# Performance work log

Measured on AMD Instinct MI355X. Metric: run time of the kernel, lower is better.

## Reference

```python
import jax, jax.numpy as jnp
import numpy as np

N_HEADS = 2
N_POINTS = 3
BN_EPS = 1e-5


def make_pe(C, D):
    # PositionalEncoding buffer, sliced to depth D: shape (D, C)
    pos = np.arange(D, dtype=np.float32)[:, None]
    div = np.exp(np.arange(0, C, 2, dtype=np.float32) * (-np.log(10000.0) / C))
    pe = np.zeros((D, C), dtype=np.float32)
    pe[:, 0::2] = np.sin(pos * div)
    pe[:, 1::2] = np.cos(pos * div)
    return jnp.asarray(pe)


def setup_inputs() -> dict:
    key = jax.random.key(0)
    b, c, zs, h, w = 2, 256, 32, 48, 48
    hp = N_HEADS * N_POINTS
    ks = jax.random.split(key, 8)
    features = jax.random.normal(ks[0], (b, c, zs, h, w), dtype=jnp.float32)
    # 1x1 Conv3d weights (out_ch, in_ch), no bias
    q_w = jax.random.normal(ks[1], (c, c), dtype=jnp.float32) * 0.05
    v_w = jax.random.normal(ks[2], (c, c), dtype=jnp.float32) * 0.05
    o_w = jax.random.normal(ks[3], (c, c), dtype=jnp.float32) * 0.05
    # sampling_offsets Linear: module inits weight=0, bias=[-1,-2,-3,1,2,3];
    # we add small random weight so sampling is input-dependent (non-degenerate)
    offs_w = jax.random.normal(ks[4], (hp, c), dtype=jnp.float32) * 0.02
    direction = np.array([[-1.0, -2.0, -3.0], [1.0, 2.0, 3.0]], dtype=np.float32)
    offs_b = jnp.asarray(direction.reshape(-1))
    attn_w = jax.random.normal(ks[5], (hp, c), dtype=jnp.float32) * 0.02
    attn_b = jax.random.normal(ks[6], (hp,), dtype=jnp.float32) * 0.1
    gamma = jnp.ones((c,), dtype=jnp.float32)
    beta = jnp.zeros((c,), dtype=jnp.float32)
    return {"features": features, "q_w": q_w, "v_w": v_w, "o_w": o_w,
            "offs_w": offs_w, "offs_b": offs_b, "attn_w": attn_w,
            "attn_b": attn_b, "gamma": gamma, "beta": beta}


def reference(features, q_w, v_w, o_w, offs_w, offs_b, attn_w, attn_b, gamma, beta):
    b, c, zs, h, w = features.shape
    pe = make_pe(c, zs)  # (zs, c)
    x = features + pe.T[None, :, :, None, None]  # (b,c,zs,h,w)
    # 1x1 conv3d == per-voxel channel GEMM
    q = jnp.einsum('oc,bcdhw->bodhw', q_w, x)
    v = jnp.einsum('oc,bcdhw->bodhw', v_w, x)
    # AdaptiveMaxPool1d(1) over h*w -> global spatial max; (b,zs,c)
    qp = jnp.transpose(q.max(axis=(3, 4)), (0, 2, 1))
    off = jnp.clip(qp @ offs_w.T + offs_b, 0.0, zs - 1)      # (b,zs,hp)
    attn = jax.nn.softmax(qp @ attn_w.T + attn_b, axis=-1)    # (b,zs,hp)
    lo = jnp.floor(off)
    hi = jnp.ceil(off)
    frac = off - lo
    # gather index depends only on (b,zs,hp), not (c,h,w): fold the
    # interp-weighted gather into a per-batch (zs_out, zs_in) mixing matrix.
    w_lo = attn * (1.0 - frac)
    w_hi = attn * frac
    oh_lo = jax.nn.one_hot(lo.astype(jnp.int32), zs, dtype=features.dtype)
    oh_hi = jax.nn.one_hot(hi.astype(jnp.int32), zs, dtype=features.dtype)
    M = (oh_lo * w_lo[..., None] + oh_hi * w_hi[..., None]).sum(axis=2)  # (b,zs,zs)
    samp = jnp.einsum('bzy,bcyhw->bczhw', M, v)  # (b,c,zs,h,w)
    out = jnp.einsum('oc,bcdhw->bodhw', o_w, samp)
    # BatchNorm3d, training-mode batch statistics (biased var), eps=1e-5
    mean = out.mean(axis=(0, 2, 3, 4))
    var = out.var(axis=(0, 2, 3, 4))
    normed = (out - mean[None, :, None, None, None]) * jax.lax.rsqrt(var + BN_EPS)[None, :, None, None, None]
    normed = normed * gamma[None, :, None, None, None] + beta[None, :, None, None, None]
    return normed + features
```

## Files before the change

### kernel.cpp

```cpp
#include <hip/hip_runtime.h>


#define B_   2
#define C_   256
#define Z_   32
#define HW_  2304
#define NSP  73728
#define NBN  147456.0f

typedef unsigned short u16;
typedef unsigned int   u32;
typedef __attribute__((ext_vector_type(8))) short bf16x8;
typedef __attribute__((ext_vector_type(4))) float f32x4;

__device__ int   g_isf32;
__device__ int   g_use_mfma;
__device__ float g_pe[Z_ * C_];
__device__ __align__(16) float g_wt[C_ * 512];
__device__ __align__(16) u16   g_afrag[32 * 8 * 2 * 64 * 8];
__device__ int   g_qmax[B_ * Z_ * C_];
__device__ __align__(16) float g_Mt[B_ * Z_ * Z_];
__device__ float g_bn_sum[C_];
__device__ float g_bn_ssq[C_];
__device__ float g_u[(size_t)B_ * C_ * NSP];

__device__ __forceinline__ u16 f2bf(float f) {
  u32 x = __float_as_uint(f);
  x = x + 0x7fffu + ((x >> 16) & 1u);
  return (u16)(x >> 16);
}
__device__ __forceinline__ float bf2f(u16 h) {
  return __uint_as_float(((u32)h) << 16);
}
__device__ __forceinline__ float ldx(const void* p, size_t i, int f32) {
  if (f32) return ((const float*)p)[i];
  return __uint_as_float(((u32)((const u16*)p)[i]) << 16);
}
__device__ __forceinline__ void stx(void* p, size_t i, int f32, float v) {
  if (f32) ((float*)p)[i] = v;
  else     ((u16*)p)[i] = f2bf(v);
}
__device__ __forceinline__ int f2key(float f) {
  int b = __float_as_int(f);
  return b >= 0 ? b : (b ^ 0x7fffffff);
}
__device__ __forceinline__ float key2f(int k) {
  int b = k >= 0 ? k : (k ^ 0x7fffffff);
  return __int_as_float(b);
}
__device__ __forceinline__ float sane(float v) {
  u32 a = __float_as_uint(v) & 0x7fffffffu;
  return (a >= 0x7f800000u) ? 0.f : v;
}
__device__ __forceinline__ float wredmax(float m) {
  m = fmaxf(m, __shfl_xor(m, 1));  m = fmaxf(m, __shfl_xor(m, 2));
  m = fmaxf(m, __shfl_xor(m, 4));  m = fmaxf(m, __shfl_xor(m, 8));
  m = fmaxf(m, __shfl_xor(m, 16)); m = fmaxf(m, __shfl_xor(m, 32));
  return m;
}
__device__ __forceinline__ float wredsum(float s) {
  s += __shfl_xor(s, 1);  s += __shfl_xor(s, 2);  s += __shfl_xor(s, 4);
  s += __shfl_xor(s, 8);  s += __shfl_xor(s, 16); s += __shfl_xor(s, 32);
  return s;
}


__device__ __forceinline__ void stage_x(const void* __restrict__ f, int f32,
                                        int b, int z, int ncol0, u16* xs) {
  const int tid = threadIdx.x;
  const int w = tid >> 6, l = tid & 63;
  const int n0 = (l & 15) * 4;
  const int g = l >> 4;
#pragma unroll
  for (int r = 0; r < 8; ++r) {
    const int k = r * 32 + w * 4 + g;
    const float pv = g_pe[z * C_ + k];
    const size_t fe = (size_t)(b * C_ + k) * NSP + ncol0 + n0;
    float x0, x1, x2, x3;
    if (f32) {
      const float4 v = *(const float4*)((const float*)f + fe);
      x0 = v.x; x1 = v.y; x2 = v.z; x3 = v.w;
    } else {
      const ushort4 v = *(const ushort4*)((const u16*)f + fe);
      x0 = bf2f(v.x); x1 = bf2f(v.y); x2 = bf2f(v.z); x3 = bf2f(v.w);
    }
    x0 += pv; x1 += pv; x2 += pv; x3 += pv;
#pragma unroll
    for (int e = 0; e < 4; ++e) {
      const float xv = (e == 0) ? x0 : (e == 1) ? x1 : (e == 2) ? x2 : x3;
      const int n = n0 + e;
      u32 byte = (u32)n * 512u + (u32)k * 2u;
      byte ^= (u32)(n & 15) << 4;
      xs[byte >> 1] = f2bf(xv);
    }
  }
}

__device__ __forceinline__ bf16x8 read_bfrag(const u16* xs, int j, int kk, int lane) {
  const int n = j * 16 + (lane & 15);
  u32 byte = (u32)n * 512u + (u32)kk * 64u + (u32)(lane >> 4) * 16u;
  byte ^= (u32)(n & 15) << 4;
  return *(const bf16x8*)(const void*)((const char*)xs + byte);
}

__device__ __forceinline__ bf16x8 load_afrag(int rs, int kk, int plane, int lane) {
  const size_t off = ((((size_t)(rs * 8 + kk) * 2 + plane) * 64 + lane) * 8);
  return *(const bf16x8*)(const void*)(g_afrag + off);
}

__global__ void k00_detect(const void* f) {
  const int t = threadIdx.x;
  u32 w = ((const u32*)f)[(size_t)t * 9973u];
  u32 e = (w >> 7) & 0xFFu;
  int in = (e >= 90u && e <= 140u) ? 1 : 0;
  for (int o = 1; o < 64; o <<= 1) in += __shfl_xor(in, o);
  if (t == 0) g_isf32 = (in < 40) ? 1 : 0;
}

__device__ __forceinline__ void pack_afrag(int row, int k, float val) {
  const int rs = row >> 4, kk = k >> 5, i = k & 7, g = (k >> 3) & 3;
  const int l = (row & 15) | (g << 4);
  u16 hi = f2bf(val);
  u16 lo = f2bf(val - bf2f(hi));
  const size_t u = (((size_t)(rs * 8 + kk) * 2) * 64 + l) * 8 + i;
  g_afrag[u] = hi;
  g_afrag[u + 512] = lo;
}

__global__ __launch_bounds__(256) void k0_setup(const void* o_w, const void* v_w,
                                                const void* q_w) {
  const int f32 = g_isf32;
  const int blk = blockIdx.x, t = threadIdx.x;
  if (blk < 256) {
    float acc = 0.f;
    for (int c = 0; c < 256; ++c)
      acc += ldx(o_w, (size_t)blk * 256 + c, f32) * ldx(v_w, (size_t)c * 256 + t, f32);
    g_wt[(size_t)t * 512 + blk] = acc;
    const float qv = ldx(q_w, (size_t)blk * 256 + t, f32);
    g_wt[(size_t)t * 512 + 256 + blk] = qv;
    pack_afrag(blk, t, acc);
    pack_afrag(256 + blk, t, qv);
  } else {
    const int ch = t;
    const float divf = expf(-(float)(ch >> 1) * (9.210340371976184f / 128.0f));
    for (int z = 0; z < Z_; ++z) {
      float arg = (float)z * divf;
      g_pe[z * 256 + ch] = (ch & 1) ? cosf(arg) : sinf(arg);
    }
    const int init_key = f2key(-1e30f);
    for (int k = t; k < B_ * Z_ * 256; k += 256) g_qmax[k] = init_key;
    g_bn_sum[t] = 0.f;
    g_bn_ssq[t] = 0.f;
  }
}

__global__ __launch_bounds__(512) void kP_probe(const void* __restrict__ f) {
  __shared__ u16 xs[16384];
  __shared__ float smacc[64][4];
  __shared__ int s_ok;
  const int f32 = g_isf32;
  if (threadIdx.x == 0) s_ok = 1;
  stage_x(f, f32, 0, 0, 0, xs);
  __syncthreads();
  if (threadIdx.x < 64) {
    const int lane = threadIdx.x;
    f32x4 acc = {0.f, 0.f, 0.f, 0.f};
    for (int kk = 0; kk < 8; ++kk) {
      bf16x8 bh = read_bfrag(xs, 0, kk, lane);
      bf16x8 ah = load_afrag(0, kk, 0, lane);
      bf16x8 al = load_afrag(0, kk, 1, lane);
      acc = __builtin_amdgcn_mfma_f32_16x16x32_bf16(ah, bh, acc, 0, 0, 0);
      acc = __builtin_amdgcn_mfma_f32_16x16x32_bf16(al, bh, acc, 0, 0, 0);
    }
#pragma unroll
    for (int reg = 0; reg < 4; ++reg) smacc[lane][reg] = acc[reg];
  }
  __syncthreads();
  if (threadIdx.x < 256) {
    const int l = threadIdx.x & 63, reg = threadIdx.x >> 6;
    const int col = l & 15;
    const int row = (l >> 4) * 4 + reg;
    float r0 = 0.f, r1 = 0.f, r2 = 0.f, r3 = 0.f;
    for (int k = 0; k < 256; k += 4) {
      r0 = fmaf(g_wt[(size_t)(k+0) * 512 + row],
                ldx(f, (size_t)(k+0) * NSP + col, f32) + g_pe[k+0], r0);
      r1 = fmaf(g_wt[(size_t)(k+1) * 512 + row],
                ldx(f, (size_t)(k+1) * NSP + col, f32) + g_pe[k+1], r1);
      r2 = fmaf(g_wt[(size_t)(k+2) * 512 + row],
                ldx(f, (size_t)(k+2) * NSP + col, f32) + g_pe[k+2], r2);
      r3 = fmaf(g_wt[(size_t)(k+3) * 512 + row],
                ldx(f, (size_t)(k+3) * NSP + col, f32) + g_pe[k+3], r3);
    }
    float ref = (r0 + r1) + (r2 + r3);
    if (!(fabsf(smacc[l][reg] - ref) <= 0.02f + 0.01f * fabsf(ref)))
      atomicAnd(&s_ok, 0);
  }
  __syncthreads();
  if (threadIdx.x == 0) g_use_mfma = s_ok;
}

__global__ __launch_bounds__(512, 4) void kA_mfma(const void* __restrict__ f) {
  if (!g_use_mfma) return;
  __shared__ u16 xs[16384];
  const int f32 = g_isf32;
  const int id = blockIdx.x;
  const int b = id / 1152;
  const int r2 = id % 1152;
  const int z = r2 / 36;
  const int m = r2 % 36;
  const int ncol0 = z * HW_ + m * 64;
  const int tid = threadIdx.x, w = tid >> 6, lane = tid & 63;

  stage_x(f, f32, b, z, ncol0, xs);
  __syncthreads();

  f32x4 acc[4][4];
  const f32x4 z4 = {0.f, 0.f, 0.f, 0.f};
#pragma unroll
  for (int r = 0; r < 4; ++r)
#pragma unroll
    for (int j = 0; j < 4; ++j) acc[r][j] = z4;

#pragma unroll 2
  for (int kk = 0; kk < 8; ++kk) {
    bf16x8 bh[4];
#pragma unroll
    for (int j = 0; j < 4; ++j) bh[j] = read_bfrag(xs, j, kk, lane);
#pragma unroll
    for (int rsl = 0; rsl < 4; ++rsl) {
      const int rs = w * 4 + rsl;
      bf16x8 ah = load_afrag(rs, kk, 0, lane);
      bf16x8 al = load_afrag(rs, kk, 1, lane);
#pragma unroll
      for (int j = 0; j < 4; ++j) {
        acc[rsl][j] = __builtin_amdgcn_mfma_f32_16x16x32_bf16(ah, bh[j], acc[rsl][j], 0, 0, 0);
        acc[rsl][j] = __builtin_amdgcn_mfma_f32_16x16x32_bf16(al, bh[j], acc[rsl][j], 0, 0, 0);
      }
    }
  }

  if (w < 4) {
#pragma unroll
    for (int rsl = 0; rsl < 4; ++rsl)
#pragma unroll
      for (int j = 0; j < 4; ++j)
#pragma unroll
        for (int reg = 0; reg < 4; ++reg) {
          const int row = (w * 4 + rsl) * 16 + (lane >> 4) * 4 + reg;
          g_u[(size_t)(b * C_ + row) * NSP + ncol0 + j * 16 + (lane & 15)] =
              acc[rsl][j][reg];
        }
  } else {
    const int rbase = (b * Z_ + z) * C_;
#pragma unroll
    for (int rsl = 0; rsl < 4; ++rsl)
#pragma unroll
      for (int reg = 0; reg < 4; ++reg) {
        float v = fmaxf(fmaxf(acc[rsl][0][reg], acc[rsl][1][reg]),
                        fmaxf(acc[rsl][2][reg], acc[rsl][3][reg]));
        v = fmaxf(v, __shfl_xor(v, 1));
        v = fmaxf(v, __shfl_xor(v, 2));
        v = fmaxf(v, __shfl_xor(v, 4));
        v = fmaxf(v, __shfl_xor(v, 8));
        if ((lane & 15) == 0)
          atomicMax(&g_qmax[rbase + ((w - 4) * 4 + rsl) * 16 + (lane >> 4) * 4 + reg],
                    f2key(v));
      }
  }
}

__global__ __launch_bounds__(256) void kA_gemm(const void* __restrict__ f) {
  if (g_use_mfma) return;
  const int f32 = g_isf32;
  const int bid = blockIdx.x;
  const int k  = bid & 7;
  const int jj = bid >> 3;
  const int T  = k + 8 * (jj >> 3);
  const int g  = jj & 7;
  const int b  = T / 288;
  const int tz = T % 288;
  const int z  = tz / 9;
  const int hc = tz % 9;
  const int t  = threadIdx.x;
  const int n_in_z = hc * 256 + t;
  const size_t fbase = (size_t)(b * C_) * NSP + (size_t)z * HW_ + n_in_z;

  float acc[64];
#pragma unroll
  for (int i = 0; i < 64; ++i) acc[i] = 0.f;

  const float* __restrict__ wtb = g_wt + g * 64;
  const float* __restrict__ pez = g_pe + z * C_;
  for (int c = 0; c < 256; ++c) {
    float fv = ldx(f, fbase + (size_t)c * NSP, f32) + pez[c];
    const float4* __restrict__ w4 = (const float4*)(wtb + (size_t)c * 512);
#pragma unroll
    for (int q = 0; q < 16; ++q) {
      float4 wv = w4[q];
      acc[4*q+0] = fmaf(wv.x, fv, acc[4*q+0]);
      acc[4*q+1] = fmaf(wv.y, fv, acc[4*q+1]);
      acc[4*q+2] = fmaf(wv.z, fv, acc[4*q+2]);
      acc[4*q+3] = fmaf(wv.w, fv, acc[4*q+3]);
    }
  }

  if (g < 4) {
    const size_t obase = (size_t)(b * C_ + g * 64) * NSP + (size_t)z * HW_ + n_in_z;
#pragma unroll
    for (int i = 0; i < 64; ++i)
      g_u[obase + (size_t)i * NSP] = acc[i];
  } else {
    const int rbase = (b * Z_ + z) * C_ + (g - 4) * 64;
#pragma unroll
    for (int i = 0; i < 64; ++i) {
      float mres = wredmax(acc[i]);
      if ((t & 63) == 0) atomicMax(&g_qmax[rbase + i], f2key(mres));
    }
  }
}

__global__ __launch_bounds__(64) void k2_mbuild(
    const void* offs_w, const void* offs_b,
    const void* attn_w, const void* attn_b) {
  const int f32 = g_isf32;
  const int bz = blockIdx.x;
  const int lane = threadIdx.x;
  float qp[4];
#pragma unroll
  for (int i = 0; i < 4; ++i)
    qp[i] = key2f(g_qmax[bz * 256 + lane * 4 + i]);

  float res[12];
  for (int p = 0; p < 12; ++p) {
    const void* wm = (p < 6) ? offs_w : attn_w;
    const size_t row = (size_t)(p < 6 ? p : p - 6) * 256;
    float s = 0.f;
#pragma unroll
    for (int i = 0; i < 4; ++i) s += qp[i] * ldx(wm, row + lane * 4 + i, f32);
    res[p] = sane(wredsum(s));
  }

  __shared__ float sm[Z_];
  if (lane < Z_) sm[lane] = 0.f;
  __syncthreads();
  if (lane == 0) {
    float att[6], mx = -1e30f;
#pragma unroll
    for (int p = 0; p < 6; ++p) {
      att[p] = sane(res[6 + p] + ldx(attn_b, p, f32));
      mx = fmaxf(mx, att[p]);
    }
    float den = 0.f;
#pragma unroll
    for (int p = 0; p < 6; ++p) { att[p] = expf(att[p] - mx); den += att[p]; }
    float inv = 1.f / den;
#pragma unroll
    for (int p = 0; p < 6; ++p) {
      float a = att[p] * inv;
      float off = sane(res[p] + ldx(offs_b, p, f32));
      off = fminf(fmaxf(off, 0.f), 31.f);
      float lo = floorf(off), hi = ceilf(off), fr = off - lo;
      int il = min(max((int)lo, 0), 31);
      int ih = min(max((int)hi, 0), 31);
      sm[il] += a * (1.f - fr);
      sm[ih] += a * fr;
    }
  }
  __syncthreads();
  if (lane < Z_) g_Mt[((bz >> 5) * Z_ + lane) * Z_ + (bz & 31)] = sm[lane];
}

__global__ __launch_bounds__(256) void kB_mix(void* outp) {
  const int f32 = g_isf32;
  const int id = blockIdx.x;
  const int b = id / 4608;
  const int rem = id % 4608;
  const int o = rem / 18;
  const int hc = rem % 18;
  const int tid = threadIdx.x, w = tid >> 6, lane = tid & 63;
  const int hw = hc * 128 + lane * 2;
  const size_t ubase = (size_t)(b * C_ + o) * NSP + hw;
  const float* __restrict__ Mtb = g_Mt + (size_t)b * Z_ * Z_ + w * 8;

  float a0[8], a1[8];
#pragma unroll
  for (int r = 0; r < 8; ++r) { a0[r] = 0.f; a1[r] = 0.f; }

  for (int y = 0; y < Z_; ++y) {
    const float2 uv = *(const float2*)(g_u + ubase + (size_t)y * HW_);
    const float4 m0 = *(const float4*)(Mtb + y * Z_);
    const float4 m1 = *(const float4*)(Mtb + y * Z_ + 4);
    a0[0] = fmaf(m0.x, uv.x, a0[0]); a1[0] = fmaf(m0.x, uv.y, a1[0]);
    a0[1] = fmaf(m0.y, uv.x, a0[1]); a1[1] = fmaf(m0.y, uv.y, a1[1]);
    a0[2] = fmaf(m0.z, uv.x, a0[2]); a1[2] = fmaf(m0.z, uv.y, a1[2]);
    a0[3] = fmaf(m0.w, uv.x, a0[3]); a1[3] = fmaf(m0.w, uv.y, a1[3]);
    a0[4] = fmaf(m1.x, uv.x, a0[4]); a1[4] = fmaf(m1.x, uv.y, a1[4]);
    a0[5] = fmaf(m1.y, uv.x, a0[5]); a1[5] = fmaf(m1.y, uv.y, a1[5]);
    a0[6] = fmaf(m1.z, uv.x, a0[6]); a1[6] = fmaf(m1.z, uv.y, a1[6]);
    a0[7] = fmaf(m1.w, uv.x, a0[7]); a1[7] = fmaf(m1.w, uv.y, a1[7]);
  }

  float s = 0.f, ss = 0.f;
  const size_t obase = (size_t)(b * C_ + o) * NSP + hw;
#pragma unroll
  for (int r = 0; r < 8; ++r) {
    const float v0 = sane(a0[r]);
    const float v1 = sane(a1[r]);
    const size_t e = obase + (size_t)(w * 8 + r) * HW_;
    if (f32) {
      *(float2*)((float*)outp + e) = make_float2(v0, v1);
    } else {
      *(u32*)((u16*)outp + e) = (u32)f2bf(v0) | ((u32)f2bf(v1) << 16);
    }
    s += v0 + v1;
    ss += v0 * v0 + v1 * v1;
  }
  s = wredsum(s);
  ss = wredsum(ss);
  if (lane == 0) {
    atomicAdd(&g_bn_sum[o], s);
    atomicAdd(&g_bn_ssq[o], ss);
  }
}

__global__ __launch_bounds__(256) void k5_final(
    const void* f, void* outp, const void* gamma, const void* beta) {
  const int f32 = g_isf32;
  const size_t e4 = ((size_t)blockIdx.x * 256 + threadIdx.x) * 4;
  const int o = (int)((e4 / NSP) & 255);
  const float mean = g_bn_sum[o] * (1.f / NBN);
  const float var = fmaxf(g_bn_ssq[o] * (1.f / NBN) - mean * mean, 0.f);
  const float rstd = rsqrtf(var + 1e-5f);
  const float sc = ldx(gamma, o, f32) * rstd;
  const float sh = ldx(beta, o, f32) - mean * sc;
  if (f32) {
    float4 ov = *(float4*)((float*)outp + e4);
    const float4 fv = *(const float4*)((const float*)f + e4);
    ov.x = sane(ov.x * sc + sh + fv.x);
    ov.y = sane(ov.y * sc + sh + fv.y);
    ov.z = sane(ov.z * sc + sh + fv.z);
    ov.w = sane(ov.w * sc + sh + fv.w);
    *(float4*)((float*)outp + e4) = ov;
  } else {
    const ushort4 ov = *(const ushort4*)((const u16*)outp + e4);
    const ushort4 fv = *(const ushort4*)((const u16*)f + e4);
    ushort4 rv;
    rv.x = f2bf(sane(bf2f(ov.x) * sc + sh + bf2f(fv.x)));
    rv.y = f2bf(sane(bf2f(ov.y) * sc + sh + bf2f(fv.y)));
    rv.z = f2bf(sane(bf2f(ov.z) * sc + sh + bf2f(fv.z)));
    rv.w = f2bf(sane(bf2f(ov.w) * sc + sh + bf2f(fv.w)));
    *(ushort4*)((u16*)outp + e4) = rv;
  }
}

extern "C" void kernel_launch(void* const* d_in, const int* in_sizes, int n_in,
                              void* d_out, int out_size, void* d_ws, size_t ws_size,
                              hipStream_t stream)
{
  (void)in_sizes; (void)n_in; (void)out_size; (void)d_ws; (void)ws_size;
  const void* f      = d_in[0];
  const void* q_w    = d_in[1];
  const void* v_w    = d_in[2];
  const void* o_w    = d_in[3];
  const void* offs_w = d_in[4];
  const void* offs_b = d_in[5];
  const void* attn_w = d_in[6];
  const void* attn_b = d_in[7];
  const void* gamma  = d_in[8];
  const void* beta   = d_in[9];

  k00_detect<<<1, 64, 0, stream>>>(f);
  k0_setup<<<257, 256, 0, stream>>>(o_w, v_w, q_w);
  kP_probe<<<1, 512, 0, stream>>>(f);
  kA_mfma<<<2304, 512, 0, stream>>>(f);
  kA_gemm<<<4608, 256, 0, stream>>>(f);
  k2_mbuild<<<64, 64, 0, stream>>>(offs_w, offs_b, attn_w, attn_b);
  kB_mix<<<9216, 256, 0, stream>>>(d_out);
  k5_final<<<36864, 256, 0, stream>>>(f, d_out, gamma, beta);
}
```

Baseline: 706.6 us.

## Store intermediate projection in bf16 and compute full z-mix per thread

The intermediate projected tensor g_u is now written as bf16 instead of fp32, which halves its write and read traffic between the GEMM kernels and the mixing kernel. The mixing kernel is restructured so that each 64-thread block has every thread compute all 32 output depths for two columns. Each u value is loaded once rather than once per wave, and the y loads are batched by eight. This lowers precision of the intermediate and raises register pressure, since each thread now holds 64 accumulators.

```diff
diff --git a/kernel.cpp b/kernel.cpp
--- a/kernel.cpp
+++ b/kernel.cpp
@@ -22,7 +22,7 @@
 __device__ __align__(16) float g_Mt[B_ * Z_ * Z_];
 __device__ float g_bn_sum[C_];
 __device__ float g_bn_ssq[C_];
-__device__ float g_u[(size_t)B_ * C_ * NSP];
+__device__ __align__(4) u16 g_u[(size_t)B_ * C_ * NSP];
 
 __device__ __forceinline__ u16 f2bf(float f) {
   u32 x = __float_as_uint(f);
@@ -35,10 +35,6 @@
 __device__ __forceinline__ float ldx(const void* p, size_t i, int f32) {
   if (f32) return ((const float*)p)[i];
   return __uint_as_float(((u32)((const u16*)p)[i]) << 16);
-}
-__device__ __forceinline__ void stx(void* p, size_t i, int f32, float v) {
-  if (f32) ((float*)p)[i] = v;
-  else     ((u16*)p)[i] = f2bf(v);
 }
 __device__ __forceinline__ int f2key(float f) {
   int b = __float_as_int(f);
@@ -248,7 +244,7 @@
         for (int reg = 0; reg < 4; ++reg) {
           const int row = (w * 4 + rsl) * 16 + (lane >> 4) * 4 + reg;
           g_u[(size_t)(b * C_ + row) * NSP + ncol0 + j * 16 + (lane & 15)] =
-              acc[rsl][j][reg];
+              f2bf(acc[rsl][j][reg]);
         }
   } else {
     const int rbase = (b * Z_ + z) * C_;
@@ -308,7 +304,7 @@
     const size_t obase = (size_t)(b * C_ + g * 64) * NSP + (size_t)z * HW_ + n_in_z;
 #pragma unroll
     for (int i = 0; i < 64; ++i)
-      g_u[obase + (size_t)i * NSP] = acc[i];
+      g_u[obase + (size_t)i * NSP] = f2bf(acc[i]);
   } else {
     const int rbase = (b * Z_ + z) * C_ + (g - 4) * 64;
 #pragma unroll
@@ -370,43 +366,58 @@
   if (lane < Z_) g_Mt[((bz >> 5) * Z_ + lane) * Z_ + (bz & 31)] = sm[lane];
 }
 
-__global__ __launch_bounds__(256) void kB_mix(void* outp) {
+__global__ __launch_bounds__(64) void kB_mix(void* outp) {
   const int f32 = g_isf32;
   const int id = blockIdx.x;
   const int b = id / 4608;
   const int rem = id % 4608;
   const int o = rem / 18;
   const int hc = rem % 18;
-  const int tid = threadIdx.x, w = tid >> 6, lane = tid & 63;
-  const int hw = hc * 128 + lane * 2;
-  const size_t ubase = (size_t)(b * C_ + o) * NSP + hw;
-  const float* __restrict__ Mtb = g_Mt + (size_t)b * Z_ * Z_ + w * 8;
-
-  float a0[8], a1[8];
-#pragma unroll
-  for (int r = 0; r < 8; ++r) { a0[r] = 0.f; a1[r] = 0.f; }
-
-  for (int y = 0; y < Z_; ++y) {
-    const float2 uv = *(const float2*)(g_u + ubase + (size_t)y * HW_);
-    const float4 m0 = *(const float4*)(Mtb + y * Z_);
-    const float4 m1 = *(const float4*)(Mtb + y * Z_ + 4);
-    a0[0] = fmaf(m0.x, uv.x, a0[0]); a1[0] = fmaf(m0.x, uv.y, a1[0]);
-    a0[1] = fmaf(m0.y, uv.x, a0[1]); a1[1] = fmaf(m0.y, uv.y, a1[1]);
-    a0[2] = fmaf(m0.z, uv.x, a0[2]); a1[2] = fmaf(m0.z, uv.y, a1[2]);
-    a0[3] = fmaf(m0.w, uv.x, a0[3]); a1[3] = fmaf(m0.w, uv.y, a1[3]);
-    a0[4] = fmaf(m1.x, uv.x, a0[4]); a1[4] = fmaf(m1.x, uv.y, a1[4]);
-    a0[5] = fmaf(m1.y, uv.x, a0[5]); a1[5] = fmaf(m1.y, uv.y, a1[5]);
-    a0[6] = fmaf(m1.z, uv.x, a0[6]); a1[6] = fmaf(m1.z, uv.y, a1[6]);
-    a0[7] = fmaf(m1.w, uv.x, a0[7]); a1[7] = fmaf(m1.w, uv.y, a1[7]);
+  const int lane = threadIdx.x;
+  const int hw = (hc * 64 + lane) * 2;
+  const u16* __restrict__ up = g_u + (size_t)(b * C_ + o) * NSP + hw;
+  const float* __restrict__ Mtb = g_Mt + (size_t)b * (Z_ * Z_);
+
+  float a0[Z_], a1[Z_];
+#pragma unroll
+  for (int zo = 0; zo < Z_; ++zo) { a0[zo] = 0.f; a1[zo] = 0.f; }
+
+#pragma unroll
+  for (int y0 = 0; y0 < Z_; y0 += 8) {
+    u32 uw0 = *(const u32*)(up + (size_t)(y0 + 0) * HW_);
+    u32 uw1 = *(const u32*)(up + (size_t)(y0 + 1) * HW_);
+    u32 uw2 = *(const u32*)(up + (size_t)(y0 + 2) * HW_);
+    u32 uw3 = *(const u32*)(up + (size_t)(y0 + 3) * HW_);
+    u32 uw4 = *(const u32*)(up + (size_t)(y0 + 4) * HW_);
+    u32 uw5 = *(const u32*)(up + (size_t)(y0 + 5) * HW_);
+    u32 uw6 = *(const u32*)(up + (size_t)(y0 + 6) * HW_);
+    u32 uw7 = *(const u32*)(up + (size_t)(y0 + 7) * HW_);
+#pragma unroll
+    for (int i = 0; i < 8; ++i) {
+      const u32 uw = (i == 0) ? uw0 : (i == 1) ? uw1 : (i == 2) ? uw2 :
+                     (i == 3) ? uw3 : (i == 4) ? uw4 : (i == 5) ? uw5 :
+                     (i == 6) ? uw6 : uw7;
+      const float x0 = bf2f((u16)(uw & 0xFFFFu));
+      const float x1 = bf2f((u16)(uw >> 16));
+      const float* __restrict__ Mr = Mtb + (y0 + i) * Z_;
+#pragma unroll
+      for (int q = 0; q < 8; ++q) {
+        const float4 mv = *(const float4*)(Mr + q * 4);
+        a0[4*q+0] = fmaf(mv.x, x0, a0[4*q+0]); a1[4*q+0] = fmaf(mv.x, x1, a1[4*q+0]);
+        a0[4*q+1] = fmaf(mv.y, x0, a0[4*q+1]); a1[4*q+1] = fmaf(mv.y, x1, a1[4*q+1]);
+        a0[4*q+2] = fmaf(mv.z, x0, a0[4*q+2]); a1[4*q+2] = fmaf(mv.z, x1, a1[4*q+2]);
+        a0[4*q+3] = fmaf(mv.w, x0, a0[4*q+3]); a1[4*q+3] = fmaf(mv.w, x1, a1[4*q+3]);
+      }
+    }
   }
 
   float s = 0.f, ss = 0.f;
   const size_t obase = (size_t)(b * C_ + o) * NSP + hw;
 #pragma unroll
-  for (int r = 0; r < 8; ++r) {
-    const float v0 = sane(a0[r]);
-    const float v1 = sane(a1[r]);
-    const size_t e = obase + (size_t)(w * 8 + r) * HW_;
+  for (int zo = 0; zo < Z_; ++zo) {
+    const float v0 = sane(a0[zo]);
+    const float v1 = sane(a1[zo]);
+    const size_t e = obase + (size_t)zo * HW_;
     if (f32) {
       *(float2*)((float*)outp + e) = make_float2(v0, v1);
     } else {
@@ -475,6 +486,6 @@
   kA_mfma<<<2304, 512, 0, stream>>>(f);
   kA_gemm<<<4608, 256, 0, stream>>>(f);
   k2_mbuild<<<64, 64, 0, stream>>>(offs_w, offs_b, attn_w, attn_b);
-  kB_mix<<<9216, 256, 0, stream>>>(d_out);
+  kB_mix<<<9216, 64, 0, stream>>>(d_out);
   k5_final<<<36864, 256, 0, stream>>>(f, d_out, gamma, beta);
 }
```

After: 785.2 us. 1.11x slower.
